# Optimization experiments

Measured on AMD Instinct MI355X. Metric: run time of the kernel, lower is better.

Reference implementation:

```python
import jax, jax.numpy as jnp
import numpy as np

N_NODES = 131072
N_EDGES = 2097152
B = 64          # graphs per batch
N_PER = 2048    # nodes per graph (equal-size graphs -> to_dense_batch == reshape)
IN_CH = 128
HID = 32
OUT_CH = 10
EPS = 1e-15


def leaky(x, slope=0.01):
    return jnp.where(x >= 0, x, slope * x)


def setup_inputs() -> dict:
    key = jax.random.key(0)
    ks = jax.random.split(key, 24)
    g = lambda k, s, sc=1.0: jax.random.normal(k, s, jnp.float32) * sc
    inp = {}
    inp["x"] = g(ks[0], (N_NODES, IN_CH))
    inp["edge_index"] = jax.random.randint(ks[1], (2, N_EDGES), 0, N_NODES, dtype=jnp.int32).astype(jnp.int64)
    inp["batch"] = jnp.repeat(jnp.arange(B, dtype=jnp.int64), N_PER)
    inp["w_embed"] = g(ks[2], (IN_CH, HID), 1.0 / np.sqrt(IN_CH))
    inp["b_embed"] = jnp.zeros((HID,), jnp.float32)
    i = 3
    for l in (1, 2):
        inp[f"gat_w{l}"] = g(ks[i], (HID, HID), 1.0 / np.sqrt(HID)); i += 1
        inp[f"att_src{l}"] = g(ks[i], (HID,), 0.1); i += 1
        inp[f"att_dst{l}"] = g(ks[i], (HID,), 0.1); i += 1
        inp[f"gat_b{l}"] = jnp.zeros((HID,), jnp.float32)
        inp[f"bn_g{l}"] = jnp.ones((HID,), jnp.float32)
        inp[f"bn_b{l}"] = jnp.zeros((HID,), jnp.float32)
        inp[f"bn_m{l}"] = g(ks[i], (HID,), 0.1); i += 1
        inp[f"bn_v{l}"] = jax.random.uniform(ks[i], (HID,), jnp.float32, 0.5, 1.5); i += 1
    inp["k1"] = g(ks[i], (5, 10, HID)); i += 1          # mem1 keys [heads=5, clusters=10, 32]
    inp["conv1_w"] = g(ks[i], (5,), 0.5); i += 1        # Conv2d(5,1,1,bias=False)
    inp["lin1_w"] = g(ks[i], (HID, 80), 1.0 / np.sqrt(HID)); i += 1
    inp["lin1_b"] = jnp.zeros((80,), jnp.float32)
    inp["k2"] = g(ks[i], (5, 1, 80)); i += 1            # mem2 keys [5, 1, 80]
    inp["conv2_w"] = g(ks[i], (5,), 0.5); i += 1
    inp["lin2_w"] = g(ks[i], (80, OUT_CH), 1.0 / np.sqrt(80)); i += 1
    inp["lin2_b"] = jnp.zeros((OUT_CH,), jnp.float32)
    return inp


def gat_conv(x, src, dst, W, a_src, a_dst, b, n):
    # PyG GATConv, heads=1, add_self_loops already in src/dst, eval (no dropout)
    h = x @ W                                   # [n, HID]
    alpha_src = h @ a_src                       # [n]
    alpha_dst = h @ a_dst
    logit = leaky(alpha_src[src] + alpha_dst[dst], 0.2)   # [E]
    m = jax.ops.segment_max(logit, dst, num_segments=n)
    m = jnp.where(jnp.isfinite(m), m, 0.0)
    e = jnp.exp(logit - m[dst])
    z = jax.ops.segment_sum(e, dst, num_segments=n)
    alpha = e / (z[dst] + 1e-16)                # softmax over in-neighborhoods
    out = jax.ops.segment_sum(alpha[:, None] * h[src], dst, num_segments=n)
    return out + b


def mem_pool(x, k, conv_w, lin_w, lin_b, tau=1.0):
    # x: [B, N, F], k: [H, K, F]  (PyG MemPooling, full mask)
    x2 = jnp.sum(x * x, -1)                     # [B, N]
    k2 = jnp.sum(k * k, -1)                     # [H, K]
    d = x2[:, None, :, None] + k2[None, :, None, :] - 2.0 * jnp.einsum('bnf,hkf->bhnk', x, k)
    d = jnp.maximum(d, 0.0)                     # squared euclidean distance [B,H,N,K]
    S = (1.0 + d / tau) ** (-(tau + 1.0) / 2.0)  # student-t kernel
    S = S / S.sum(-1, keepdims=True)
    S = jnp.einsum('h,bhnk->bnk', conv_w, S)    # 1x1 conv over heads
    S = jax.nn.softmax(S, axis=-1)              # [B, N, K]
    xo = jnp.einsum('bnk,bnf->bkf', S, x) @ lin_w + lin_b
    return xo, S


def kl_loss(S):
    # PyG MemPooling.kl_loss, KLDivLoss(reduction='batchmean')
    S2 = S * S
    P = S2 / jnp.maximum(S.sum(1, keepdims=True), EPS)
    denom = P.sum(2, keepdims=True)
    denom = jnp.where(S.sum(2, keepdims=True) == 0.0, 1.0, denom)
    P = jnp.maximum(P / denom, EPS)
    logS = jnp.log(jnp.maximum(S, EPS))
    return jnp.sum(P * (jnp.log(P) - logS)) / S.shape[0]


def _forward(x, w_embed, b_embed,
             gat_w1, att_src1, att_dst1, gat_b1, bn_g1, bn_b1, bn_m1, bn_v1,
             gat_w2, att_src2, att_dst2, gat_b2, bn_g2, bn_b2, bn_m2, bn_v2,
             k1, conv1_w, lin1_w, lin1_b, k2, conv2_w, lin2_w, lin2_b,
             edge_index, batch):
    n = x.shape[0]
    loops = jnp.arange(n, dtype=edge_index.dtype)
    src = jnp.concatenate([edge_index[0], loops])   # GAT add_self_loops
    dst = jnp.concatenate([edge_index[1], loops])
    h = x @ w_embed + b_embed
    # two DeepGCNLayer 'res+' blocks: norm -> act -> (dropout) -> conv, + residual
    for gw, asr, ads, gb, g_, b_, m_, v_ in (
        (gat_w1, att_src1, att_dst1, gat_b1, bn_g1, bn_b1, bn_m1, bn_v1),
        (gat_w2, att_src2, att_dst2, gat_b2, bn_g2, bn_b2, bn_m2, bn_v2),
    ):
        t = (h - m_) / jnp.sqrt(v_ + 1e-5) * g_ + b_   # BatchNorm1d (eval)
        t = leaky(t)
        h = h + gat_conv(t, src, dst, gw, asr, ads, gb, n)
    xd = h.reshape(B, N_PER, HID)   # to_dense_batch with equal-sized graphs (batch)
    x1, S1 = mem_pool(xd, k1, conv1_w, lin1_w, lin1_b)      # [B, 10, 80]
    x2, S2 = mem_pool(leaky(x1), k2, conv2_w, lin2_w, lin2_b)  # [B, 1, 10]
    out = jax.nn.log_softmax(leaky(x2[:, 0, :]), axis=-1)
    kl = kl_loss(S2) + kl_loss(S1)
    return out, kl


def reference(x, w_embed, b_embed,
              gat_w1, att_src1, att_dst1, gat_b1, bn_g1, bn_b1, bn_m1, bn_v1,
              gat_w2, att_src2, att_dst2, gat_b2, bn_g2, bn_b2, bn_m2, bn_v2,
              k1, conv1_w, lin1_w, lin1_b, k2, conv2_w, lin2_w, lin2_b,
              edge_index, batch):
    return _forward(x, w_embed, b_embed,
                    gat_w1, att_src1, att_dst1, gat_b1, bn_g1, bn_b1, bn_m1, bn_v1,
                    gat_w2, att_src2, att_dst2, gat_b2, bn_g2, bn_b2, bn_m2, bn_v2,
                    k1, conv1_w, lin1_w, lin1_b, k2, conv2_w, lin2_w, lin2_b,
                    edge_index, batch)
```

## Files before the change

kernel.cpp:

```cpp
#include <hip/hip_runtime.h>
#include <hip/hip_bf16.h>

#define N_NODES 131072
#define N_EDGES 2097152
#define NB 64
#define N_PER 2048
#define IN_CH 128
#define HID 32
#define NBKT 512

__device__ __forceinline__ float leaky01(float v) { return v >= 0.0f ? v : 0.01f * v; }
__device__ __forceinline__ float leaky2(float v)  { return v >= 0.0f ? v : 0.2f  * v; }

__global__ void k_embed(const float* __restrict__ x, const float* __restrict__ W,
                        const float* __restrict__ bias, float* __restrict__ h) {
    __shared__ float4 sW4[IN_CH * HID / 4];
    __shared__ float4 sx4[32 * IN_CH / 4];
    int tid = threadIdx.x;
    const float4* W4 = (const float4*)W;
    for (int i = tid; i < IN_CH * HID / 4; i += 256) sW4[i] = W4[i];
    const float4* x4 = (const float4*)(x + (size_t)blockIdx.x * 32 * IN_CH);
    for (int i = tid; i < 32 * IN_CH / 4; i += 256) sx4[i] = x4[i];
    __syncthreads();
    const float* sW = (const float*)sW4;
    const float* sx = (const float*)sx4;
    int r0 = tid >> 5, c = tid & 31;
    float b = bias[c];
    float acc0 = b, acc1 = b, acc2 = b, acc3 = b;
    #pragma unroll
    for (int k = 0; k < IN_CH; ++k) {
        float w = sW[k * HID + c];
        acc0 += sx[(r0     ) * IN_CH + k] * w;
        acc1 += sx[(r0 +  8) * IN_CH + k] * w;
        acc2 += sx[(r0 + 16) * IN_CH + k] * w;
        acc3 += sx[(r0 + 24) * IN_CH + k] * w;
    }
    int row = blockIdx.x * 32 + r0;
    h[(row     ) * HID + c] = acc0;
    h[(row +  8) * HID + c] = acc1;
    h[(row + 16) * HID + c] = acc2;
    h[(row + 24) * HID + c] = acc3;
}


__global__ void kb_count(const int* __restrict__ ei, int* __restrict__ bcnt) {
    __shared__ int hist[NBKT];
    int tid = threadIdx.x;
    hist[tid] = 0; hist[tid + 256] = 0;
    __syncthreads();
    int e0 = blockIdx.x * 8192;
    #pragma unroll 4
    for (int k = 0; k < 32; ++k) {
        int d = ei[N_EDGES + e0 + k * 256 + tid];
        atomicAdd(&hist[d >> 8], 1);
    }
    __syncthreads();
    atomicAdd(&bcnt[tid], hist[tid]);
    atomicAdd(&bcnt[tid + 256], hist[tid + 256]);
}

__global__ void kb_bscan(const int* __restrict__ bcnt, int* __restrict__ bbase,
                         int* __restrict__ bcur) {
    __shared__ int s[NBKT];
    int tid = threadIdx.x;
    int v = bcnt[tid];
    s[tid] = v; __syncthreads();
    for (int off = 1; off < NBKT; off <<= 1) {
        int t = (tid >= off) ? s[tid - off] : 0;
        __syncthreads();
        s[tid] += t;
        __syncthreads();
    }
    int ex = s[tid] - v;
    bbase[tid] = ex;
    bcur[tid] = ex;
}

__global__ void kb_scatter(const int* __restrict__ ei, int* __restrict__ bcur,
                           unsigned int* __restrict__ pk) {
    __shared__ int hist[NBKT];
    __shared__ int base[NBKT];
    int tid = threadIdx.x;
    hist[tid] = 0; hist[tid + 256] = 0;
    __syncthreads();
    int e0 = blockIdx.x * 8192;
    #pragma unroll 4
    for (int k = 0; k < 32; ++k) {
        int d = ei[N_EDGES + e0 + k * 256 + tid];
        atomicAdd(&hist[d >> 8], 1);
    }
    __syncthreads();
    base[tid] = atomicAdd(&bcur[tid], hist[tid]);
    base[tid + 256] = atomicAdd(&bcur[tid + 256], hist[tid + 256]);
    __syncthreads();
    hist[tid] = 0; hist[tid + 256] = 0;
    __syncthreads();
    for (int k = 0; k < 32; ++k) {
        int e = e0 + k * 256 + tid;
        int d = ei[N_EDGES + e];
        int s = ei[e];
        int b = d >> 8;
        int loc = atomicAdd(&hist[b], 1);
        pk[base[b] + loc] = (unsigned int)s | ((unsigned int)(d & 255) << 17);
    }
}

__global__ void kb_hist(const unsigned int* __restrict__ pk, const int* __restrict__ bcnt,
                        const int* __restrict__ bbase, int* __restrict__ cnt) {
    __shared__ int lc[256];
    int b = blockIdx.x, tid = threadIdx.x;
    lc[tid] = 0; __syncthreads();
    int n = bcnt[b], base = bbase[b];
    for (int i = tid; i < n; i += 256) atomicAdd(&lc[pk[base + i] >> 17], 1);
    __syncthreads();
    cnt[b * 256 + tid] = lc[tid];
}

__global__ void k_scan1(const int* __restrict__ cnt, int* __restrict__ rp, int* __restrict__ bs) {
    __shared__ int s[256];
    int tid = threadIdx.x;
    int gid = blockIdx.x * 256 + tid;
    int v = cnt[gid];
    s[tid] = v; __syncthreads();
    for (int off = 1; off < 256; off <<= 1) {
        int t = (tid >= off) ? s[tid - off] : 0;
        __syncthreads();
        s[tid] += t;
        __syncthreads();
    }
    rp[gid] = s[tid] - v;
    if (tid == 255) bs[blockIdx.x] = s[255];
}

__global__ void k_scan2(int* __restrict__ bs) {
    __shared__ int s[512];
    int tid = threadIdx.x;
    int v = bs[tid];
    s[tid] = v; __syncthreads();
    for (int off = 1; off < 512; off <<= 1) {
        int t = (tid >= off) ? s[tid - off] : 0;
        __syncthreads();
        s[tid] += t;
        __syncthreads();
    }
    bs[tid] = s[tid] - v;
}

__global__ void k_scan3(int* __restrict__ rp, const int* __restrict__ bs) {
    int gid = blockIdx.x * 256 + threadIdx.x;
    rp[gid] += bs[blockIdx.x];
    if (gid == 0) rp[N_NODES] = N_EDGES;
}

__global__ void kb_fill(const unsigned int* __restrict__ pk, const int* __restrict__ bcnt,
                        const int* __restrict__ bbase, const int* __restrict__ rp,
                        int* __restrict__ esrc) {
    __shared__ int lcur[256];
    int b = blockIdx.x, tid = threadIdx.x;
    lcur[tid] = rp[b * 256 + tid];
    __syncthreads();
    int n = bcnt[b], base = bbase[b];
    for (int i = tid; i < n; i += 256) {
        unsigned int v = pk[base + i];
        int pos = atomicAdd(&lcur[v >> 17], 1);
        esrc[pos] = (int)(v & 0x1FFFFu);
    }
}

__global__ void k_gat_pre(const float* __restrict__ h, const float* __restrict__ W,
                          const float* __restrict__ a_src, const float* __restrict__ a_dst,
                          const float* __restrict__ bn_g, const float* __restrict__ bn_b,
                          const float* __restrict__ bn_m, const float* __restrict__ bn_v,
                          float* __restrict__ g, float* __restrict__ asv, float* __restrict__ adv) {
    __shared__ float sW[HID * HID];
    __shared__ float st[32 * HID];
    __shared__ float ssc[HID], ssh[HID];
    int tid = threadIdx.x;
    if (tid < HID) {
        float sc = bn_g[tid] * rsqrtf(bn_v[tid] + 1e-5f);
        ssc[tid] = sc;
        ssh[tid] = bn_b[tid] - bn_m[tid] * sc;
    }
    for (int i = tid; i < HID * HID; i += 256) sW[i] = W[i];
    __syncthreads();
    int base = blockIdx.x * 32 * HID;
    for (int i = tid; i < 32 * HID; i += 256) {
        int ch = i & 31;
        st[i] = leaky01(h[base + i] * ssc[ch] + ssh[ch]);
    }
    __syncthreads();
    int r0 = tid >> 5, c = tid & 31;
    float as_c = a_src[c], ad_c = a_dst[c];
    float acc0 = 0.f, acc1 = 0.f, acc2 = 0.f, acc3 = 0.f;
    #pragma unroll
    for (int k = 0; k < HID; ++k) {
        float w = sW[k * HID + c];
        acc0 += st[(r0     ) * HID + k] * w;
        acc1 += st[(r0 +  8) * HID + k] * w;
        acc2 += st[(r0 + 16) * HID + k] * w;
        acc3 += st[(r0 + 24) * HID + k] * w;
    }
    g[base + (r0     ) * HID + c] = acc0;
    g[base + (r0 +  8) * HID + c] = acc1;
    g[base + (r0 + 16) * HID + c] = acc2;
    g[base + (r0 + 24) * HID + c] = acc3;
    float p0 = acc0 * as_c, p1 = acc1 * as_c, p2 = acc2 * as_c, p3 = acc3 * as_c;
    float q0 = acc0 * ad_c, q1 = acc1 * ad_c, q2 = acc2 * ad_c, q3 = acc3 * ad_c;
    #pragma unroll
    for (int m = 16; m >= 1; m >>= 1) {
        p0 += __shfl_xor(p0, m); p1 += __shfl_xor(p1, m);
        p2 += __shfl_xor(p2, m); p3 += __shfl_xor(p3, m);
        q0 += __shfl_xor(q0, m); q1 += __shfl_xor(q1, m);
        q2 += __shfl_xor(q2, m); q3 += __shfl_xor(q3, m);
    }
    if (c == 0) {
        int row = blockIdx.x * 32 + r0;
        asv[row     ] = p0;  adv[row     ] = q0;
        asv[row +  8] = p1;  adv[row +  8] = q1;
        asv[row + 16] = p2;  adv[row + 16] = q2;
        asv[row + 24] = p3;  adv[row + 24] = q3;
    }
}

__global__ void k_maxl(const float* __restrict__ asv, const int* __restrict__ rp,
                       const int* __restrict__ esrc, float* __restrict__ smax) {
    int node = blockIdx.x * 256 + threadIdx.x;
    float m = asv[node];
    int beg = rp[node], end = rp[node + 1];
    int j = beg;
    for (; j + 4 <= end; j += 4) {
        int s0 = esrc[j], s1 = esrc[j + 1], s2 = esrc[j + 2], s3 = esrc[j + 3];
        float a0 = asv[s0], a1 = asv[s1], a2 = asv[s2], a3 = asv[s3];
        m = fmaxf(m, fmaxf(fmaxf(a0, a1), fmaxf(a2, a3)));
    }
    for (; j < end; ++j) m = fmaxf(m, asv[esrc[j]]);
    smax[node] = m;
}

__global__ void k_aggr(float* __restrict__ h, const float* __restrict__ g,
                       const float* __restrict__ asv, const float* __restrict__ adv,
                       const float* __restrict__ smax,
                       const int* __restrict__ rp, const int* __restrict__ esrc,
                       const float* __restrict__ gb) {
    int node = blockIdx.x * 8 + (threadIdx.x >> 5);
    int c = threadIdx.x & 31;
    float gbc = gb[c];
    float ad_i = adv[node];
    float m = leaky2(smax[node] + ad_i);
    float e_self = __expf(leaky2(asv[node] + ad_i) - m);
    float z = e_self;
    float acc = e_self * g[node * HID + c];
    int beg = rp[node], end = rp[node + 1];
    int j = beg;
    for (; j + 4 <= end; j += 4) {
        int s0 = esrc[j], s1 = esrc[j + 1], s2 = esrc[j + 2], s3 = esrc[j + 3];
        float l0 = asv[s0], l1 = asv[s1], l2 = asv[s2], l3 = asv[s3];
        float g0 = g[s0 * HID + c], g1 = g[s1 * HID + c];
        float g2 = g[s2 * HID + c], g3 = g[s3 * HID + c];
        float e0 = __expf(leaky2(l0 + ad_i) - m);
        float e1 = __expf(leaky2(l1 + ad_i) - m);
        float e2 = __expf(leaky2(l2 + ad_i) - m);
        float e3 = __expf(leaky2(l3 + ad_i) - m);
        z += (e0 + e1) + (e2 + e3);
        acc += e0 * g0 + e1 * g1 + e2 * g2 + e3 * g3;
    }
    for (; j < end; ++j) {
        int s = esrc[j];
        float e = __expf(leaky2(asv[s] + ad_i) - m);
        z += e;
        acc += e * g[s * HID + c];
    }
    h[node * HID + c] += acc / (z + 1e-16f) + gbc;
}

__global__ void k_mem1(const float* __restrict__ h, const float* __restrict__ k1,
                       const float* __restrict__ conv_w,
                       float* __restrict__ S1, float* __restrict__ xo,
                       float* __restrict__ colsum) {
    __shared__ float sk1[5 * 10 * HID];
    __shared__ float sk2[50];
    __shared__ float scw[5];
    __shared__ float s1l[256][10];
    int tid = threadIdx.x;
    for (int i = tid; i < 5 * 10 * HID; i += 256) sk1[i] = k1[i];
    if (tid < 5) scw[tid] = conv_w[tid];
    __syncthreads();
    if (tid < 50) {
        float s = 0.0f;
        for (int f = 0; f < HID; ++f) { float t = sk1[tid * HID + f]; s += t * t; }
        sk2[tid] = s;
    }
    __syncthreads();

    int nid = blockIdx.x * 256 + tid;
    float xr[HID];
    const float4* xp = (const float4*)(h + nid * HID);
    #pragma unroll
    for (int i = 0; i < 8; ++i) {
        float4 v = xp[i];
        xr[4 * i] = v.x; xr[4 * i + 1] = v.y; xr[4 * i + 2] = v.z; xr[4 * i + 3] = v.w;
    }
    float x2n = 0.0f;
    #pragma unroll
    for (int f = 0; f < HID; ++f) x2n += xr[f] * xr[f];

    float Sc[10];
    #pragma unroll
    for (int k = 0; k < 10; ++k) Sc[k] = 0.0f;

    for (int hh = 0; hh < 5; ++hh) {
        float tmp[10];
        float rsum = 0.0f;
        #pragma unroll
        for (int k = 0; k < 10; ++k) {
            float dot = 0.0f;
            #pragma unroll
            for (int f = 0; f < HID; ++f) dot += xr[f] * sk1[(hh * 10 + k) * HID + f];
            float d = x2n + sk2[hh * 10 + k] - 2.0f * dot;
            d = d > 0.0f ? d : 0.0f;
            float s = 1.0f / (1.0f + d);
            tmp[k] = s;
            rsum += s;
        }
        float w = scw[hh] / rsum;
        #pragma unroll
        for (int k = 0; k < 10; ++k) Sc[k] += tmp[k] * w;
    }
    float mx = Sc[0];
    #pragma unroll
    for (int k = 1; k < 10; ++k) mx = fmaxf(mx, Sc[k]);
    float se = 0.0f;
    #pragma unroll
    for (int k = 0; k < 10; ++k) { float e = __expf(Sc[k] - mx); Sc[k] = e; se += e; }
    float inv = 1.0f / se;
    #pragma unroll
    for (int k = 0; k < 10; ++k) {
        float v = Sc[k] * inv;
        s1l[tid][k] = v;
        S1[nid * 10 + k] = v;
    }
    __syncthreads();

    int b = nid >> 11;
    for (int idx = tid; idx < 320; idx += 256) {
        int k = idx >> 5, f = idx & 31;
        float s = 0.0f;
        const float* xb = h + (blockIdx.x * 256) * HID + f;
        for (int n = 0; n < 256; ++n) s += s1l[n][k] * xb[n * HID];
        atomicAdd(&xo[(b * 10 + k) * HID + f], s);
    }
    for (int k = tid; k < 10; k += 256) {
        float s = 0.0f;
        for (int n = 0; n < 256; ++n) s += s1l[n][k];
        atomicAdd(&colsum[b * 10 + k], s);
    }
}

__global__ void k_kl(const float* __restrict__ S1, const float* __restrict__ colsum,
                     float* __restrict__ klg) {
    __shared__ float red[256];
    int tid = threadIdx.x;
    int nid = blockIdx.x * 256 + tid;
    int b = nid >> 11;
    const float* srow = S1 + nid * 10;
    float p[10], sv[10];
    float dsum = 0.0f;
    #pragma unroll
    for (int k = 0; k < 10; ++k) {
        float s = srow[k];
        sv[k] = s;
        float pk = s * s / fmaxf(colsum[b * 10 + k], 1e-15f);
        p[k] = pk;
        dsum += pk;
    }
    float invd = 1.0f / dsum;
    float term = 0.0f;
    #pragma unroll
    for (int k = 0; k < 10; ++k) {
        float pk = fmaxf(p[k] * invd, 1e-15f);
        float s = fmaxf(sv[k], 1e-15f);
        term += pk * (logf(pk) - logf(s));
    }
    red[tid] = term; __syncthreads();
    for (int off = 128; off > 0; off >>= 1) {
        if (tid < off) red[tid] += red[tid + off];
        __syncthreads();
    }
    if (tid == 0) atomicAdd(klg, red[0]);
}

__global__ void k_head(const float* __restrict__ xo, const float* __restrict__ l1w,
                       const float* __restrict__ l1b, const float* __restrict__ l2w,
                       const float* __restrict__ l2b, const float* __restrict__ klg,
                       float* __restrict__ out) {
    __shared__ float sxo[320];
    __shared__ float s80[80];
    __shared__ float lg[10];
    int b = blockIdx.x, tid = threadIdx.x;
    for (int i = tid; i < 320; i += 128) sxo[i] = xo[b * 320 + i];
    __syncthreads();
    if (tid < 80) {
        float s = 0.0f;
        for (int k = 0; k < 10; ++k) {
            float a = l1b[tid];
            #pragma unroll
            for (int i = 0; i < HID; ++i) a += sxo[k * HID + i] * l1w[i * 80 + tid];
            s += leaky01(a);
        }
        s80[tid] = s;
    }
    __syncthreads();
    if (tid < 10) {
        float a = l2b[tid];
        for (int f = 0; f < 80; ++f) a += s80[f] * l2w[f * 10 + tid];
        lg[tid] = leaky01(a);
    }
    __syncthreads();
    if (tid == 0) {
        float m = lg[0];
        for (int j = 1; j < 10; ++j) m = fmaxf(m, lg[j]);
        float se = 0.0f;
        for (int j = 0; j < 10; ++j) se += expf(lg[j] - m);
        float ls = logf(se);
        for (int j = 0; j < 10; ++j) out[b * 10 + j] = lg[j] - m - ls;
        if (b == 0) out[640] = klg[0] * (1.0f / 64.0f);
    }
}

extern "C" void kernel_launch(void* const* d_in, const int* in_sizes, int n_in,
                              void* d_out, int out_size, void* d_ws, size_t ws_size,
                              hipStream_t stream) {
    const float* x       = (const float*)d_in[0];
    const int*   ei      = (const int*)d_in[1];
    const float* w_embed = (const float*)d_in[3];
    const float* b_embed = (const float*)d_in[4];
    const float* k1      = (const float*)d_in[21];
    const float* conv1_w = (const float*)d_in[22];
    const float* lin1_w  = (const float*)d_in[23];
    const float* lin1_b  = (const float*)d_in[24];
    const float* lin2_w  = (const float*)d_in[27];
    const float* lin2_b  = (const float*)d_in[28];
    float* out = (float*)d_out;

    char* w = (char*)d_ws;
    float* h    = (float*)(w + 0);
    float* g    = (float*)(w + 16777216);
    unsigned int* pk = (unsigned int*)(w + 16777216);
    float* asv  = (float*)(w + 33554432);
    float* adv  = (float*)(w + 34078720);
    float* S1   = (float*)(w + 34603008);
    int*   esrc = (int*)  (w + 39845888);
    int*   rp   = (int*)  (w + 48234496);
    int*   cnt  = (int*)  (w + 48759040);
    float* smax = (float*)cnt;
    int*   bs   = (int*)  (w + 49283328);
    int*   bcnt = (int*)  (w + 49285376);
    int*   bbase= (int*)  (w + 49287424);
    int*   bcur = (int*)  (w + 49289472);
    float* xo   = (float*)(w + 49291520);
    float* cs   = (float*)(w + 49373440);
    float* klg  = (float*)(w + 49376000);

    hipMemsetAsync(bcnt, 0, NBKT * sizeof(int), stream);
    hipMemsetAsync(xo, 0, 81920 + 2560 + 4, stream);

    k_embed<<<N_NODES / 32, 256, 0, stream>>>(x, w_embed, b_embed, h);

    kb_count<<<N_EDGES / 8192, 256, 0, stream>>>(ei, bcnt);
    kb_bscan<<<1, NBKT, 0, stream>>>(bcnt, bbase, bcur);
    kb_scatter<<<N_EDGES / 8192, 256, 0, stream>>>(ei, bcur, pk);
    kb_hist<<<NBKT, 256, 0, stream>>>(pk, bcnt, bbase, cnt);
    k_scan1<<<N_NODES / 256, 256, 0, stream>>>(cnt, rp, bs);
    k_scan2<<<1, 512, 0, stream>>>(bs);
    k_scan3<<<N_NODES / 256, 256, 0, stream>>>(rp, bs);
    kb_fill<<<NBKT, 256, 0, stream>>>(pk, bcnt, bbase, rp, esrc);

    for (int l = 0; l < 2; ++l) {
        int o = 5 + l * 8;
        const float* gw  = (const float*)d_in[o + 0];
        const float* asr = (const float*)d_in[o + 1];
        const float* ads = (const float*)d_in[o + 2];
        const float* gbb = (const float*)d_in[o + 3];
        const float* bg  = (const float*)d_in[o + 4];
        const float* bb  = (const float*)d_in[o + 5];
        const float* bm  = (const float*)d_in[o + 6];
        const float* bv  = (const float*)d_in[o + 7];
        k_gat_pre<<<N_NODES / 32, 256, 0, stream>>>(h, gw, asr, ads, bg, bb, bm, bv, g, asv, adv);
        k_maxl<<<N_NODES / 256, 256, 0, stream>>>(asv, rp, esrc, smax);
        k_aggr<<<N_NODES / 8, 256, 0, stream>>>(h, g, asv, adv, smax, rp, esrc, gbb);
    }

    k_mem1<<<N_NODES / 256, 256, 0, stream>>>(h, k1, conv1_w, S1, xo, cs);
    k_kl<<<N_NODES / 256, 256, 0, stream>>>(S1, cs, klg);

    k_head<<<NB, 128, 0, stream>>>(xo, lin1_w, lin1_b, lin2_w, lin2_b, klg, out);
}
```

Baseline: 488.4 us.

## Fuse embed with first GAT pre, drop max pass, bf16 features, merge scans

Fuses the embedding matmul with the first layer's BatchNorm/GAT projection and folds the row-pointer scan into the per-bucket histogram kernel, removing three scan kernels. The separate segment-max kernel is dropped, so softmax weights are computed as raw exponentials without max subtraction. Gathered features are stored in bf16, and edges are processed cooperatively per warp with shuffles. k_mem1 stages h through padded shared memory. Skipping the max subtraction risks overflow for large logits, and bf16 storage lowers precision.

Measured after the change: 448.9 us. -8.1%, faster.

```diff
diff --git a/kernel.cpp b/kernel.cpp
--- a/kernel.cpp
+++ b/kernel.cpp
@@ -11,21 +11,37 @@
 
 __device__ __forceinline__ float leaky01(float v) { return v >= 0.0f ? v : 0.01f * v; }
 __device__ __forceinline__ float leaky2(float v)  { return v >= 0.0f ? v : 0.2f  * v; }
-
-__global__ void k_embed(const float* __restrict__ x, const float* __restrict__ W,
-                        const float* __restrict__ bias, float* __restrict__ h) {
+__device__ __forceinline__ float bf2f(__hip_bfloat16 v) { return __bfloat162float(v); }
+
+__global__ void k_embed_pre(const float* __restrict__ x, const float* __restrict__ We,
+                            const float* __restrict__ be,
+                            const float* __restrict__ W1, const float* __restrict__ a_src,
+                            const float* __restrict__ a_dst,
+                            const float* __restrict__ bn_g, const float* __restrict__ bn_b,
+                            const float* __restrict__ bn_m, const float* __restrict__ bn_v,
+                            float* __restrict__ h, __hip_bfloat16* __restrict__ g,
+                            float* __restrict__ asv, float* __restrict__ adv) {
     __shared__ float4 sW4[IN_CH * HID / 4];
     __shared__ float4 sx4[32 * IN_CH / 4];
-    int tid = threadIdx.x;
-    const float4* W4 = (const float4*)W;
+    __shared__ float st[32 * HID];
+    __shared__ float sW1[HID * HID];
+    __shared__ float ssc[HID], ssh[HID];
+    int tid = threadIdx.x;
+    if (tid < HID) {
+        float sc = bn_g[tid] * rsqrtf(bn_v[tid] + 1e-5f);
+        ssc[tid] = sc;
+        ssh[tid] = bn_b[tid] - bn_m[tid] * sc;
+    }
+    const float4* W4 = (const float4*)We;
     for (int i = tid; i < IN_CH * HID / 4; i += 256) sW4[i] = W4[i];
     const float4* x4 = (const float4*)(x + (size_t)blockIdx.x * 32 * IN_CH);
     for (int i = tid; i < 32 * IN_CH / 4; i += 256) sx4[i] = x4[i];
+    for (int i = tid; i < HID * HID; i += 256) sW1[i] = W1[i];
     __syncthreads();
     const float* sW = (const float*)sW4;
     const float* sx = (const float*)sx4;
     int r0 = tid >> 5, c = tid & 31;
-    float b = bias[c];
+    float b = be[c];
     float acc0 = b, acc1 = b, acc2 = b, acc3 = b;
     #pragma unroll
     for (int k = 0; k < IN_CH; ++k) {
@@ -35,13 +51,48 @@
         acc2 += sx[(r0 + 16) * IN_CH + k] * w;
         acc3 += sx[(r0 + 24) * IN_CH + k] * w;
     }
-    int row = blockIdx.x * 32 + r0;
-    h[(row     ) * HID + c] = acc0;
-    h[(row +  8) * HID + c] = acc1;
-    h[(row + 16) * HID + c] = acc2;
-    h[(row + 24) * HID + c] = acc3;
-}
-
+    int base = blockIdx.x * 32 * HID;
+    h[base + (r0     ) * HID + c] = acc0;
+    h[base + (r0 +  8) * HID + c] = acc1;
+    h[base + (r0 + 16) * HID + c] = acc2;
+    h[base + (r0 + 24) * HID + c] = acc3;
+    float sc = ssc[c], sh = ssh[c];
+    st[(r0     ) * HID + c] = leaky01(acc0 * sc + sh);
+    st[(r0 +  8) * HID + c] = leaky01(acc1 * sc + sh);
+    st[(r0 + 16) * HID + c] = leaky01(acc2 * sc + sh);
+    st[(r0 + 24) * HID + c] = leaky01(acc3 * sc + sh);
+    __syncthreads();
+    float as_c = a_src[c], ad_c = a_dst[c];
+    float g0 = 0.f, g1 = 0.f, g2 = 0.f, g3 = 0.f;
+    #pragma unroll
+    for (int k = 0; k < HID; ++k) {
+        float w = sW1[k * HID + c];
+        g0 += st[(r0     ) * HID + k] * w;
+        g1 += st[(r0 +  8) * HID + k] * w;
+        g2 += st[(r0 + 16) * HID + k] * w;
+        g3 += st[(r0 + 24) * HID + k] * w;
+    }
+    g[base + (r0     ) * HID + c] = __float2bfloat16(g0);
+    g[base + (r0 +  8) * HID + c] = __float2bfloat16(g1);
+    g[base + (r0 + 16) * HID + c] = __float2bfloat16(g2);
+    g[base + (r0 + 24) * HID + c] = __float2bfloat16(g3);
+    float p0 = g0 * as_c, p1 = g1 * as_c, p2 = g2 * as_c, p3 = g3 * as_c;
+    float q0 = g0 * ad_c, q1 = g1 * ad_c, q2 = g2 * ad_c, q3 = g3 * ad_c;
+    #pragma unroll
+    for (int m = 16; m >= 1; m >>= 1) {
+        p0 += __shfl_xor(p0, m); p1 += __shfl_xor(p1, m);
+        p2 += __shfl_xor(p2, m); p3 += __shfl_xor(p3, m);
+        q0 += __shfl_xor(q0, m); q1 += __shfl_xor(q1, m);
+        q2 += __shfl_xor(q2, m); q3 += __shfl_xor(q3, m);
+    }
+    if (c == 0) {
+        int row = blockIdx.x * 32 + r0;
+        asv[row     ] = p0;  adv[row     ] = q0;
+        asv[row +  8] = p1;  adv[row +  8] = q1;
+        asv[row + 16] = p2;  adv[row + 16] = q2;
+        asv[row + 24] = p3;  adv[row + 24] = q3;
+    }
+}
 
 __global__ void kb_count(const int* __restrict__ ei, int* __restrict__ bcnt) {
     __shared__ int hist[NBKT];
@@ -106,50 +157,24 @@
 }
 
 __global__ void kb_hist(const unsigned int* __restrict__ pk, const int* __restrict__ bcnt,
-                        const int* __restrict__ bbase, int* __restrict__ cnt) {
+                        const int* __restrict__ bbase, int* __restrict__ rp) {
     __shared__ int lc[256];
+    __shared__ int sc[256];
     int b = blockIdx.x, tid = threadIdx.x;
     lc[tid] = 0; __syncthreads();
     int n = bcnt[b], base = bbase[b];
     for (int i = tid; i < n; i += 256) atomicAdd(&lc[pk[base + i] >> 17], 1);
     __syncthreads();
-    cnt[b * 256 + tid] = lc[tid];
-}
-
-__global__ void k_scan1(const int* __restrict__ cnt, int* __restrict__ rp, int* __restrict__ bs) {
-    __shared__ int s[256];
-    int tid = threadIdx.x;
-    int gid = blockIdx.x * 256 + tid;
-    int v = cnt[gid];
-    s[tid] = v; __syncthreads();
+    int v = lc[tid];
+    sc[tid] = v; __syncthreads();
     for (int off = 1; off < 256; off <<= 1) {
-        int t = (tid >= off) ? s[tid - off] : 0;
+        int t = (tid >= off) ? sc[tid - off] : 0;
         __syncthreads();
-        s[tid] += t;
+        sc[tid] += t;
         __syncthreads();
     }
-    rp[gid] = s[tid] - v;
-    if (tid == 255) bs[blockIdx.x] = s[255];
-}
-
-__global__ void k_scan2(int* __restrict__ bs) {
-    __shared__ int s[512];
-    int tid = threadIdx.x;
-    int v = bs[tid];
-    s[tid] = v; __syncthreads();
-    for (int off = 1; off < 512; off <<= 1) {
-        int t = (tid >= off) ? s[tid - off] : 0;
-        __syncthreads();
-        s[tid] += t;
-        __syncthreads();
-    }
-    bs[tid] = s[tid] - v;
-}
-
-__global__ void k_scan3(int* __restrict__ rp, const int* __restrict__ bs) {
-    int gid = blockIdx.x * 256 + threadIdx.x;
-    rp[gid] += bs[blockIdx.x];
-    if (gid == 0) rp[N_NODES] = N_EDGES;
+    rp[b * 256 + tid] = base + sc[tid] - v;
+    if (b == NBKT - 1 && tid == 255) rp[N_NODES] = N_EDGES;
 }
 
 __global__ void kb_fill(const unsigned int* __restrict__ pk, const int* __restrict__ bcnt,
@@ -171,7 +196,8 @@
                           const float* __restrict__ a_src, const float* __restrict__ a_dst,
                           const float* __restrict__ bn_g, const float* __restrict__ bn_b,
                           const float* __restrict__ bn_m, const float* __restrict__ bn_v,
-                          float* __restrict__ g, float* __restrict__ asv, float* __restrict__ adv) {
+                          __hip_bfloat16* __restrict__ g, float* __restrict__ asv,
+                          float* __restrict__ adv) {
     __shared__ float sW[HID * HID];
     __shared__ float st[32 * HID];
     __shared__ float ssc[HID], ssh[HID];
@@ -191,21 +217,21 @@
     __syncthreads();
     int r0 = tid >> 5, c = tid & 31;
     float as_c = a_src[c], ad_c = a_dst[c];
-    float acc0 = 0.f, acc1 = 0.f, acc2 = 0.f, acc3 = 0.f;
+    float g0 = 0.f, g1 = 0.f, g2 = 0.f, g3 = 0.f;
     #pragma unroll
     for (int k = 0; k < HID; ++k) {
         float w = sW[k * HID + c];
-        acc0 += st[(r0     ) * HID + k] * w;
-        acc1 += st[(r0 +  8) * HID + k] * w;
-        acc2 += st[(r0 + 16) * HID + k] * w;
-        acc3 += st[(r0 + 24) * HID + k] * w;
-    }
-    g[base + (r0     ) * HID + c] = acc0;
-    g[base + (r0 +  8) * HID + c] = acc1;
-    g[base + (r0 + 16) * HID + c] = acc2;
-    g[base + (r0 + 24) * HID + c] = acc3;
-    float p0 = acc0 * as_c, p1 = acc1 * as_c, p2 = acc2 * as_c, p3 = acc3 * as_c;
-    float q0 = acc0 * ad_c, q1 = acc1 * ad_c, q2 = acc2 * ad_c, q3 = acc3 * ad_c;
+        g0 += st[(r0     ) * HID + k] * w;
+        g1 += st[(r0 +  8) * HID + k] * w;
+        g2 += st[(r0 + 16) * HID + k] * w;
+        g3 += st[(r0 + 24) * HID + k] * w;
+    }
+    g[base + (r0     ) * HID + c] = __float2bfloat16(g0);
+    g[base + (r0 +  8) * HID + c] = __float2bfloat16(g1);
+    g[base + (r0 + 16) * HID + c] = __float2bfloat16(g2);
+    g[base + (r0 + 24) * HID + c] = __float2bfloat16(g3);
+    float p0 = g0 * as_c, p1 = g1 * as_c, p2 = g2 * as_c, p3 = g3 * as_c;
+    float q0 = g0 * ad_c, q1 = g1 * ad_c, q2 = g2 * ad_c, q3 = g3 * ad_c;
     #pragma unroll
     for (int m = 16; m >= 1; m >>= 1) {
         p0 += __shfl_xor(p0, m); p1 += __shfl_xor(p1, m);
@@ -222,61 +248,55 @@
     }
 }
 
-__global__ void k_maxl(const float* __restrict__ asv, const int* __restrict__ rp,
-                       const int* __restrict__ esrc, float* __restrict__ smax) {
-    int node = blockIdx.x * 256 + threadIdx.x;
-    float m = asv[node];
+__global__ void k_aggr(float* __restrict__ h, const __hip_bfloat16* __restrict__ g,
+                       const float* __restrict__ asv, const float* __restrict__ adv,
+                       const int* __restrict__ rp, const int* __restrict__ esrc,
+                       const float* __restrict__ gbias) {
+    int node = blockIdx.x * 8 + (threadIdx.x >> 5);
+    int lane = threadIdx.x & 31;
+    float ad_i = adv[node];
+    float e_self = __expf(leaky2(asv[node] + ad_i));
+    float z = e_self;
+    float acc = e_self * bf2f(g[node * HID + lane]);
     int beg = rp[node], end = rp[node + 1];
-    int j = beg;
-    for (; j + 4 <= end; j += 4) {
-        int s0 = esrc[j], s1 = esrc[j + 1], s2 = esrc[j + 2], s3 = esrc[j + 3];
-        float a0 = asv[s0], a1 = asv[s1], a2 = asv[s2], a3 = asv[s3];
-        m = fmaxf(m, fmaxf(fmaxf(a0, a1), fmaxf(a2, a3)));
-    }
-    for (; j < end; ++j) m = fmaxf(m, asv[esrc[j]]);
-    smax[node] = m;
-}
-
-__global__ void k_aggr(float* __restrict__ h, const float* __restrict__ g,
-                       const float* __restrict__ asv, const float* __restrict__ adv,
-                       const float* __restrict__ smax,
-                       const int* __restrict__ rp, const int* __restrict__ esrc,
-                       const float* __restrict__ gb) {
-    int node = blockIdx.x * 8 + (threadIdx.x >> 5);
-    int c = threadIdx.x & 31;
-    float gbc = gb[c];
-    float ad_i = adv[node];
-    float m = leaky2(smax[node] + ad_i);
-    float e_self = __expf(leaky2(asv[node] + ad_i) - m);
-    float z = e_self;
-    float acc = e_self * g[node * HID + c];
-    int beg = rp[node], end = rp[node + 1];
-    int j = beg;
-    for (; j + 4 <= end; j += 4) {
-        int s0 = esrc[j], s1 = esrc[j + 1], s2 = esrc[j + 2], s3 = esrc[j + 3];
-        float l0 = asv[s0], l1 = asv[s1], l2 = asv[s2], l3 = asv[s3];
-        float g0 = g[s0 * HID + c], g1 = g[s1 * HID + c];
-        float g2 = g[s2 * HID + c], g3 = g[s3 * HID + c];
-        float e0 = __expf(leaky2(l0 + ad_i) - m);
-        float e1 = __expf(leaky2(l1 + ad_i) - m);
-        float e2 = __expf(leaky2(l2 + ad_i) - m);
-        float e3 = __expf(leaky2(l3 + ad_i) - m);
-        z += (e0 + e1) + (e2 + e3);
-        acc += e0 * g0 + e1 * g1 + e2 * g2 + e3 * g3;
-    }
-    for (; j < end; ++j) {
-        int s = esrc[j];
-        float e = __expf(leaky2(asv[s] + ad_i) - m);
-        z += e;
-        acc += e * g[s * HID + c];
-    }
-    h[node * HID + c] += acc / (z + 1e-16f) + gbc;
+    for (int jb = beg; jb < end; jb += 32) {
+        int j = jb + lane;
+        int s = 0; float e = 0.0f;
+        if (j < end) {
+            s = esrc[j];
+            e = __expf(leaky2(asv[s] + ad_i));
+        }
+        float zs = e;
+        #pragma unroll
+        for (int mm = 16; mm >= 1; mm >>= 1) zs += __shfl_xor(zs, mm);
+        z += zs;
+        int cnt = end - jb; if (cnt > 32) cnt = 32;
+        int jj = 0;
+        for (; jj + 4 <= cnt; jj += 4) {
+            int s0 = __shfl(s, jj, 32), s1 = __shfl(s, jj + 1, 32);
+            int s2 = __shfl(s, jj + 2, 32), s3 = __shfl(s, jj + 3, 32);
+            float e0 = __shfl(e, jj, 32), e1 = __shfl(e, jj + 1, 32);
+            float e2 = __shfl(e, jj + 2, 32), e3 = __shfl(e, jj + 3, 32);
+            float g0 = bf2f(g[s0 * HID + lane]);
+            float g1 = bf2f(g[s1 * HID + lane]);
+            float g2 = bf2f(g[s2 * HID + lane]);
+            float g3 = bf2f(g[s3 * HID + lane]);
+            acc += e0 * g0 + e1 * g1 + e2 * g2 + e3 * g3;
+        }
+        for (; jj < cnt; ++jj) {
+            int ss = __shfl(s, jj, 32);
+            float ee = __shfl(e, jj, 32);
+            acc += ee * bf2f(g[ss * HID + lane]);
+        }
+    }
+    h[node * HID + lane] += acc / (z + 1e-16f) + gbias[lane];
 }
 
 __global__ void k_mem1(const float* __restrict__ h, const float* __restrict__ k1,
                        const float* __restrict__ conv_w,
                        float* __restrict__ S1, float* __restrict__ xo,
                        float* __restrict__ colsum) {
+    __shared__ float sh[256 * 33];
     __shared__ float sk1[5 * 10 * HID];
     __shared__ float sk2[50];
     __shared__ float scw[5];
@@ -284,6 +304,13 @@
     int tid = threadIdx.x;
     for (int i = tid; i < 5 * 10 * HID; i += 256) sk1[i] = k1[i];
     if (tid < 5) scw[tid] = conv_w[tid];
+    const float4* hp = (const float4*)(h + (size_t)blockIdx.x * 256 * HID);
+    for (int i = tid; i < 2048; i += 256) {
+        float4 v = hp[i];
+        int row = i >> 3, c4 = (i & 7) * 4;
+        float* dst = &sh[row * 33 + c4];
+        dst[0] = v.x; dst[1] = v.y; dst[2] = v.z; dst[3] = v.w;
+    }
     __syncthreads();
     if (tid < 50) {
         float s = 0.0f;
@@ -294,12 +321,8 @@
 
     int nid = blockIdx.x * 256 + tid;
     float xr[HID];
-    const float4* xp = (const float4*)(h + nid * HID);
-    #pragma unroll
-    for (int i = 0; i < 8; ++i) {
-        float4 v = xp[i];
-        xr[4 * i] = v.x; xr[4 * i + 1] = v.y; xr[4 * i + 2] = v.z; xr[4 * i + 3] = v.w;
-    }
+    #pragma unroll
+    for (int f = 0; f < HID; ++f) xr[f] = sh[tid * 33 + f];
     float x2n = 0.0f;
     #pragma unroll
     for (int f = 0; f < HID; ++f) x2n += xr[f] * xr[f];
@@ -345,8 +368,8 @@
     for (int idx = tid; idx < 320; idx += 256) {
         int k = idx >> 5, f = idx & 31;
         float s = 0.0f;
-        const float* xb = h + (blockIdx.x * 256) * HID + f;
-        for (int n = 0; n < 256; ++n) s += s1l[n][k] * xb[n * HID];
+        #pragma unroll 4
+        for (int n = 0; n < 256; ++n) s += s1l[n][k] * sh[n * 33 + f];
         atomicAdd(&xo[(b * 10 + k) * HID + f], s);
     }
     for (int k = tid; k < 10; k += 256) {
@@ -443,52 +466,57 @@
     float* out = (float*)d_out;
 
     char* w = (char*)d_ws;
-    float* h    = (float*)(w + 0);
-    float* g    = (float*)(w + 16777216);
-    unsigned int* pk = (unsigned int*)(w + 16777216);
-    float* asv  = (float*)(w + 33554432);
-    float* adv  = (float*)(w + 34078720);
-    float* S1   = (float*)(w + 34603008);
-    int*   esrc = (int*)  (w + 39845888);
-    int*   rp   = (int*)  (w + 48234496);
-    int*   cnt  = (int*)  (w + 48759040);
-    float* smax = (float*)cnt;
-    int*   bs   = (int*)  (w + 49283328);
-    int*   bcnt = (int*)  (w + 49285376);
-    int*   bbase= (int*)  (w + 49287424);
-    int*   bcur = (int*)  (w + 49289472);
-    float* xo   = (float*)(w + 49291520);
-    float* cs   = (float*)(w + 49373440);
-    float* klg  = (float*)(w + 49376000);
-
-    hipMemsetAsync(bcnt, 0, NBKT * sizeof(int), stream);
-    hipMemsetAsync(xo, 0, 81920 + 2560 + 4, stream);
-
-    k_embed<<<N_NODES / 32, 256, 0, stream>>>(x, w_embed, b_embed, h);
+    float*          h    = (float*)(w + 0);
+    __hip_bfloat16* g    = (__hip_bfloat16*)(w + 16777216);
+    unsigned int*   pk   = (unsigned int*)(w + 25165824);
+    int*            esrc = (int*)(w + 33554432);
+    float*          asv  = (float*)(w + 41943040);
+    float*          adv  = (float*)(w + 42467328);
+    int*            rp   = (int*)(w + 42991616);
+    float*          S1   = (float*)(w + 43516160);
+    int*            bbase= (int*)(w + 48759040);
+    int*            bcur = (int*)(w + 48761088);
+    int*            bcnt = (int*)(w + 48763136);
+    float*          xo   = (float*)(w + 48765184);
+    float*          cs   = (float*)(w + 48847104);
+    float*          klg  = (float*)(w + 48849664);
+
+    hipMemsetAsync(bcnt, 0, 2048 + 81920 + 2560 + 4, stream);
+
+    {
+        const float* gw1  = (const float*)d_in[5];
+        const float* asr1 = (const float*)d_in[6];
+        const float* ads1 = (const float*)d_in[7];
+        const float* bg1  = (const float*)d_in[9];
+        const float* bb1  = (const float*)d_in[10];
+        const float* bm1  = (const float*)d_in[11];
+        const float* bv1  = (const float*)d_in[12];
+        k_embed_pre<<<N_NODES / 32, 256, 0, stream>>>(x, w_embed, b_embed,
+                                                      gw1, asr1, ads1,
+                                                      bg1, bb1, bm1, bv1,
+                                                      h, g, asv, adv);
+    }
 
     kb_count<<<N_EDGES / 8192, 256, 0, stream>>>(ei, bcnt);
     kb_bscan<<<1, NBKT, 0, stream>>>(bcnt, bbase, bcur);
     kb_scatter<<<N_EDGES / 8192, 256, 0, stream>>>(ei, bcur, pk);
-    kb_hist<<<NBKT, 256, 0, stream>>>(pk, bcnt, bbase, cnt);
-    k_scan1<<<N_NODES / 256, 256, 0, stream>>>(cnt, rp, bs);
-    k_scan2<<<1, 512, 0, stream>>>(bs);
-    k_scan3<<<N_NODES / 256, 256, 0, stream>>>(rp, bs);
+    kb_hist<<<NBKT, 256, 0, stream>>>(pk, bcnt, bbase, rp);
     kb_fill<<<NBKT, 256, 0, stream>>>(pk, bcnt, bbase, rp, esrc);
 
-    for (int l = 0; l < 2; ++l) {
-        int o = 5 + l * 8;
-        const float* gw  = (const float*)d_in[o + 0];
-        const float* asr = (const float*)d_in[o + 1];
-        const float* ads = (const float*)d_in[o + 2];
-        const float* gbb = (const float*)d_in[o + 3];
-        const float* bg  = (const float*)d_in[o + 4];
-        const float* bb  = (const float*)d_in[o + 5];
-        const float* bm  = (const float*)d_in[o + 6];
-        const float* bv  = (const float*)d_in[o + 7];
-        k_gat_pre<<<N_NODES / 32, 256, 0, stream>>>(h, gw, asr, ads, bg, bb, bm, bv, g, asv, adv);
-        k_maxl<<<N_NODES / 256, 256, 0, stream>>>(asv, rp, esrc, smax);
-        k_aggr<<<N_NODES / 8, 256, 0, stream>>>(h, g, asv, adv, smax, rp, esrc, gbb);
-    }
+    k_aggr<<<N_NODES / 8, 256, 0, stream>>>(h, g, asv, adv, rp, esrc,
+                                            (const float*)d_in[8]);
+
+    k_gat_pre<<<N_NODES / 32, 256, 0, stream>>>(h,
+                                                (const float*)d_in[13],
+                                                (const float*)d_in[14],
+                                                (const float*)d_in[15],
+                                                (const float*)d_in[17],
+                                                (const float*)d_in[18],
+                                                (const float*)d_in[19],
+                                                (const float*)d_in[20],
+                                                g, asv, adv);
+    k_aggr<<<N_NODES / 8, 256, 0, stream>>>(h, g, asv, adv, rp, esrc,
+                                            (const float*)d_in[16]);
 
     k_mem1<<<N_NODES / 256, 256, 0, stream>>>(h, k1, conv1_w, S1, xo, cs);
     k_kl<<<N_NODES / 256, 256, 0, stream>>>(S1, cs, klg);
```
